# Kernel tuning notes

Hardware: AMD Instinct MI355X
Metric: run time of the kernel (lower is better)

Reference implementation:

```python
import jax, jax.numpy as jnp
import numpy as np

Nmax = 200
B = 512
LATENT = 128
ENC_H = 256
DEC_H = 512
M = 20


def setup_inputs() -> dict:
    key = jax.random.key(0)
    ks = jax.random.split(key, 16)

    def rn(k, shape):
        return jax.random.normal(k, shape, jnp.float32) / np.sqrt(shape[0]).astype(np.float32)

    inp = {}
    inp["x"] = jax.random.normal(ks[0], (Nmax + 1, B, 5), jnp.float32)
    inp["N_s"] = jax.random.randint(ks[1], (B, 1), 0, Nmax, jnp.int32)
    inp["eps"] = jax.random.normal(ks[2], (B, LATENT), jnp.float32)
    # bidirectional encoder LSTM (torch gate order i,f,g,o)
    inp["enc_Wih_f"] = rn(ks[3], (5, 4 * ENC_H))
    inp["enc_Whh_f"] = rn(ks[4], (ENC_H, 4 * ENC_H))
    inp["enc_b_f"] = jnp.zeros((4 * ENC_H,), jnp.float32)
    inp["enc_Wih_b"] = rn(ks[5], (5, 4 * ENC_H))
    inp["enc_Whh_b"] = rn(ks[6], (ENC_H, 4 * ENC_H))
    inp["enc_b_b"] = jnp.zeros((4 * ENC_H,), jnp.float32)
    inp["W_mu"] = rn(ks[7], (2 * ENC_H, LATENT))
    inp["b_mu"] = jnp.zeros((LATENT,), jnp.float32)
    inp["W_logvar"] = rn(ks[8], (2 * ENC_H, LATENT))
    inp["b_logvar"] = jnp.zeros((LATENT,), jnp.float32)
    # decoder
    inp["W_fc_in"] = rn(ks[9], (LATENT, 2 * DEC_H))
    inp["b_fc_in"] = jnp.zeros((2 * DEC_H,), jnp.float32)
    inp["dec_Wih"] = rn(ks[10], (5 + LATENT, 4 * DEC_H))
    inp["dec_Whh"] = rn(ks[11], (DEC_H, 4 * DEC_H))
    inp["dec_b"] = jnp.zeros((4 * DEC_H,), jnp.float32)
    inp["W_out"] = rn(ks[12], (DEC_H, 6 * M + 3))
    inp["b_out"] = jnp.zeros((6 * M + 3,), jnp.float32)
    return inp


def _lstm_step(h, c, x, Wih, Whh, b):
    g = x @ Wih + h @ Whh + b
    i, f, gg, o = jnp.split(g, 4, axis=-1)
    c = jax.nn.sigmoid(f) * c + jax.nn.sigmoid(i) * jnp.tanh(gg)
    h = jax.nn.sigmoid(o) * jnp.tanh(c)
    return h, c


def reference(x, N_s, eps, enc_Wih_f, enc_Whh_f, enc_b_f, enc_Wih_b, enc_Whh_b, enc_b_b,
              W_mu, b_mu, W_logvar, b_logvar, W_fc_in, b_fc_in,
              dec_Wih, dec_Whh, dec_b, W_out, b_out):
    Bn = x.shape[1]
    dt = x.dtype

    # ---- bidirectional LSTM encoder -> mean, logvar ----
    def run(xs, Wih, Whh, b):
        H = Whh.shape[0]
        def step(hc, xt):
            h, c = _lstm_step(hc[0], hc[1], xt, Wih, Whh, b)
            return (h, c), None
        (h, _), _ = jax.lax.scan(step, (jnp.zeros((Bn, H), dt), jnp.zeros((Bn, H), dt)), xs)
        return h

    h_enc = jnp.concatenate([run(x, enc_Wih_f, enc_Whh_f, enc_b_f),
                             run(x[::-1], enc_Wih_b, enc_Whh_b, enc_b_b)], axis=-1)
    mean = h_enc @ W_mu + b_mu
    logvar = h_enc @ W_logvar + b_logvar
    z = mean + jnp.exp(logvar / 2) * eps  # reparameterize

    # decoder initial state from z
    hc0 = jnp.tanh(z @ W_fc_in + b_fc_in)
    h0, c0 = jnp.split(hc0, 2, axis=-1)

    # ---- make_target ----
    lens = N_s[:, 0]  # [B]
    mask = (jnp.arange(Nmax + 1)[:, None] < lens[None, :]).astype(dt)  # [Nmax+1, B]
    dx, dy = x[..., 0], x[..., 1]

    stroke0 = jnp.broadcast_to(jnp.array([0, 0, 1, 0, 0], dt), (Bn, 5))  # SOS
    empty = jnp.array([0, 0, 0, 0, 1], dt)
    steps = jnp.arange(1, Nmax)
    xs = (x[1:Nmax], dx[1:Nmax], dy[1:Nmax], mask[1:Nmax], steps)

    def step(carry, inp):
        h, c, prev, pl, ol = carry
        xt, dxt, dyt, mt, i = inp
        h, c = _lstm_step(h, c, jnp.concatenate([prev, z], axis=-1), dec_Wih, dec_Whh, dec_b)
        y = h @ W_out + b_out  # [B, 6M+3]
        mix = y[:, :6 * M].reshape(Bn, M, 6)
        pi_h, mu_x, mu_y, sx_h, sy_h, rho_h = (mix[..., j] for j in range(6))
        q_h = y[:, 6 * M:]
        pi = jax.nn.softmax(pi_h, axis=-1)
        sx, sy, rho = jnp.exp(sx_h), jnp.exp(sy_h), jnp.tanh(rho_h)
        # pen reconstruction loss (categorical CE over p1,p2,p3)
        pl = pl + (-(xt[:, 2:] * jax.nn.log_softmax(q_h, axis=-1)).sum() / Bn) / Nmax
        # offset reconstruction loss (bivariate GMM NLL, masked)
        zx = (dxt[:, None] - mu_x) / sx
        zy = (dyt[:, None] - mu_y) / sy
        om = 1.0 - rho * rho
        pdf = jnp.exp(-(zx * zx + zy * zy - 2.0 * rho * zx * zy) / (2.0 * om)) / (2.0 * jnp.pi * sx * sy * jnp.sqrt(om))
        gmm = (pi * pdf).sum(axis=-1)
        ol = ol + (-(mt * jnp.log(gmm + 1e-6)).sum() / Bn) / Nmax
        # deterministic next stroke: expected offsets + argmax pen state
        q = jax.nn.softmax(q_h, axis=-1)
        stroke = jnp.concatenate([(pi * mu_x).sum(-1, keepdims=True),
                                  (pi * mu_y).sum(-1, keepdims=True),
                                  jax.nn.one_hot(jnp.argmax(q, axis=-1), 3, dtype=dt)], axis=-1)
        stroke = jnp.where((i > lens)[:, None], empty, stroke)  # per-index stroke masking
        return (h, c, stroke, pl, ol), stroke

    init = (h0, c0, stroke0, jnp.zeros((), dt), jnp.zeros((), dt))
    (_, _, _, pen_loss, offset_loss), strokes = jax.lax.scan(step, init, xs)
    # torch returns strokes[1:]; row Nmax is never written -> zeros
    strokes = jnp.concatenate([strokes, jnp.zeros((1, Bn, 5), dt)], axis=0)  # [Nmax, B, 5]
    return strokes, offset_loss, pen_loss, mean, logvar
```

## Files before the change

### kernel.cpp

```cpp
#include <hip/hip_runtime.h>
#include <hip/hip_bf16.h>
#include <math.h>

#define NMAX 200
#define BATCH 512
#define EH 256
#define DH 512
#define NMIX 20
#define HE_BLK 131072
#define HD_BLK 262144

typedef unsigned short u16;
typedef __bf16 bfx8 __attribute__((ext_vector_type(8)));
typedef float  fx4  __attribute__((ext_vector_type(4)));
typedef u16    us8  __attribute__((ext_vector_type(8)));

__device__ __forceinline__ float sigm(float x) { return 1.0f / (1.0f + __expf(-x)); }
__device__ __forceinline__ u16 f2bf(float x) {
    unsigned u = __float_as_uint(x);
    unsigned r = u + 0x7fffu + ((u >> 16) & 1u);
    return (u16)(r >> 16);
}
__device__ __forceinline__ float bf2f(u16 h) { return __uint_as_float(((unsigned)h) << 16); }

__device__ __forceinline__ int ldsidx(int r, int k) { return r * 64 + (k ^ ((r & 7) << 3)); }

__device__ __forceinline__ void stageA(u16* As, const u16* src, int stride) {
    int t = threadIdx.x;
    int r = t >> 3, k0 = (t & 7) * 8;
    *(us8*)&As[ldsidx(r, k0)] = *(const us8*)&src[r * stride + k0];
}
__device__ __forceinline__ void stageB(u16* Bs, const u16* wT, int K, int GS, int j0, int kbase) {
#pragma unroll
    for (int i = 0; i < 4; ++i) {
        int idx = i * 256 + threadIdx.x;
        int r = idx >> 3, k0 = (idx & 7) * 8;
        int n = (r >> 5) * GS + j0 + (r & 31);
        *(us8*)&Bs[ldsidx(r, k0)] = *(const us8*)&wT[n * K + kbase + k0];
    }
}

__device__ __forceinline__ void gemm_chunk(const u16* As_hi, const u16* As_lo,
                                           const u16* Bs_hi, const u16* Bs_lo,
                                           int wv, int lane, fx4 acc[2][2]) {
    const int ar = lane & 15, kg = (lane >> 4) * 8;
#pragma unroll
    for (int ks = 0; ks < 2; ++ks) {
        const int kk = ks * 32 + kg;
        bfx8 ah[2], al[2], bh[2], bl[2];
#pragma unroll
        for (int mt = 0; mt < 2; ++mt) {
            int r = mt * 16 + ar;
            int idx = ldsidx(r, kk);
            ah[mt] = *(const bfx8*)&As_hi[idx];
            al[mt] = *(const bfx8*)&As_lo[idx];
        }
#pragma unroll
        for (int nt = 0; nt < 2; ++nt) {
            int r = wv * 32 + nt * 16 + ar;
            int idx = ldsidx(r, kk);
            bh[nt] = *(const bfx8*)&Bs_hi[idx];
            bl[nt] = *(const bfx8*)&Bs_lo[idx];
        }
#pragma unroll
        for (int mt = 0; mt < 2; ++mt)
#pragma unroll
            for (int nt = 0; nt < 2; ++nt) {
                acc[mt][nt] = __builtin_amdgcn_mfma_f32_16x16x32_bf16(ah[mt], bh[nt], acc[mt][nt], 0, 0, 0);
                acc[mt][nt] = __builtin_amdgcn_mfma_f32_16x16x32_bf16(ah[mt], bl[nt], acc[mt][nt], 0, 0, 0);
                acc[mt][nt] = __builtin_amdgcn_mfma_f32_16x16x32_bf16(al[mt], bh[nt], acc[mt][nt], 0, 0, 0);
            }
    }
}

__global__ __launch_bounds__(256) void prep_split_T(const float* __restrict__ src,
                                                    u16* dhi, u16* dlo, int K, int Nsrc, int Nout) {
    int idx = blockIdx.x * 256 + threadIdx.x;
    if (idx >= Nout * K) return;
    int n = idx / K, k = idx - n * K;
    float v = (n < Nsrc) ? src[k * Nsrc + n] : 0.0f;
    u16 hh = f2bf(v);
    dhi[idx] = hh;
    dlo[idx] = f2bf(v - bf2f(hh));
}

__global__ __launch_bounds__(256) void enc_step_m(
    const float* __restrict__ x,
    const float* __restrict__ Wih_f, const float* __restrict__ b_f,
    const float* __restrict__ Wih_b, const float* __restrict__ b_b,
    const u16* whhT,
    u16* he,
    float* c_base,
    int t)
{
    const int dir = blockIdx.z;
    const int j0 = blockIdx.x * 32;
    const int row0 = blockIdx.y * 32;
    const int pb = t & 1, nb = pb ^ 1;
    const int ts = dir ? (NMAX - t) : t;
    const float* Wih  = dir ? Wih_b : Wih_f;
    const float* bias = dir ? b_b : b_f;
    const u16* wT_hi = whhT + (dir * 2 + 0) * 262144;
    const u16* wT_lo = whhT + (dir * 2 + 1) * 262144;
    const u16* hp_hi = he + ((pb * 2 + dir) * 2 + 0) * HE_BLK;
    const u16* hp_lo = he + ((pb * 2 + dir) * 2 + 1) * HE_BLK;
    u16* hn_hi = he + ((nb * 2 + dir) * 2 + 0) * HE_BLK;
    u16* hn_lo = he + ((nb * 2 + dir) * 2 + 1) * HE_BLK;
    float* c = c_base + dir * 131072;

    __shared__ __align__(16) char smem[40960];
    u16* As_hi = (u16*)smem;
    u16* As_lo = As_hi + 2048;
    u16* Bs_hi = As_lo + 2048;
    u16* Bs_lo = Bs_hi + 8192;
    float (*gL)[32][32] = (float(*)[32][32])(smem + 8192);
    __shared__ float xL[32][5];
    __shared__ float WihL[5][128];
    __shared__ float biasL[128];

    const int tid = threadIdx.x;
    const int wv = tid >> 6, lane = tid & 63;
    if (tid < 160) { int r = tid / 5, i = tid % 5; xL[r][i] = x[ts * 2560 + (row0 + r) * 5 + i]; }
    if (tid < 128) {
        biasL[tid] = bias[(tid >> 5) * 256 + j0 + (tid & 31)];
#pragma unroll
        for (int i = 0; i < 5; ++i) WihL[i][tid] = Wih[i * 1024 + (tid >> 5) * 256 + j0 + (tid & 31)];
    }

    fx4 acc[2][2] = {};
    for (int ch = 0; ch < 4; ++ch) {
        if (ch) __syncthreads();
        const int kb = ch * 64;
        stageA(As_hi, hp_hi + row0 * 256 + kb, 256);
        stageA(As_lo, hp_lo + row0 * 256 + kb, 256);
        stageB(Bs_hi, wT_hi, 256, 256, j0, kb);
        stageB(Bs_lo, wT_lo, 256, 256, j0, kb);
        __syncthreads();
        gemm_chunk(As_hi, As_lo, Bs_hi, Bs_lo, wv, lane, acc);
    }
    __syncthreads();
#pragma unroll
    for (int mt = 0; mt < 2; ++mt)
#pragma unroll
        for (int nt = 0; nt < 2; ++nt)
#pragma unroll
            for (int r2 = 0; r2 < 4; ++r2)
                gL[wv][mt * 16 + (lane >> 4) * 4 + r2][nt * 16 + (lane & 15)] = acc[mt][nt][r2];
    __syncthreads();

    {
        const int j = tid & 31, rq = tid >> 5;
#pragma unroll
        for (int ii = 0; ii < 4; ++ii) {
            const int b = rq + ii * 8;
            float gv[4];
#pragma unroll
            for (int g = 0; g < 4; ++g) {
                float s = gL[g][b][j] + biasL[g * 32 + j];
#pragma unroll
                for (int i = 0; i < 5; ++i) s += xL[b][i] * WihL[i][g * 32 + j];
                gv[g] = s;
            }
            const int gidx = (row0 + b) * 256 + j0 + j;
            float cv = c[gidx];
            cv = sigm(gv[1]) * cv + sigm(gv[0]) * tanhf(gv[2]);
            c[gidx] = cv;
            float hv = sigm(gv[3]) * tanhf(cv);
            u16 hh = f2bf(hv);
            hn_hi[gidx] = hh;
            hn_lo[gidx] = f2bf(hv - bf2f(hh));
        }
    }
}

__global__ __launch_bounds__(256) void latent1(
    const u16* he,
    const float* __restrict__ W_mu, const float* __restrict__ b_mu,
    const float* __restrict__ W_lv, const float* __restrict__ b_lv,
    const float* __restrict__ eps, float* z, float* out)
{
    __shared__ float hs[16 * 512];
    const int row0 = blockIdx.x * 16;
    const int tid = threadIdx.x;
    const u16* hf_hi = he + ((1 * 2 + 0) * 2 + 0) * HE_BLK;
    const u16* hf_lo = he + ((1 * 2 + 0) * 2 + 1) * HE_BLK;
    const u16* hb_hi = he + ((1 * 2 + 1) * 2 + 0) * HE_BLK;
    const u16* hb_lo = he + ((1 * 2 + 1) * 2 + 1) * HE_BLK;
    for (int i = tid; i < 8192; i += 256) {
        int r = i >> 9, col = i & 511;
        int gi = (row0 + r) * 256;
        float v;
        if (col < 256) v = bf2f(hf_hi[gi + col]) + bf2f(hf_lo[gi + col]);
        else { int cc = col - 256; v = bf2f(hb_hi[gi + cc]) + bf2f(hb_lo[gi + cc]); }
        hs[i] = v;
    }
    __syncthreads();
    for (int p = tid; p < 2048; p += 256) {
        int r = p >> 7, cc = p & 127;
        const float* hr = hs + r * 512;
        float m = 0, lv = 0;
#pragma unroll 8
        for (int k = 0; k < 512; ++k) {
            float hv = hr[k];
            m  += hv * W_mu[k * 128 + cc];
            lv += hv * W_lv[k * 128 + cc];
        }
        m += b_mu[cc]; lv += b_lv[cc];
        int b = row0 + r;
        out[512002 + b * 128 + cc] = m;
        out[577538 + b * 128 + cc] = lv;
        z[b * 128 + cc] = m + __expf(0.5f * lv) * eps[b * 128 + cc];
    }
}

__global__ __launch_bounds__(256) void latent2(
    const float* __restrict__ z, const float* __restrict__ W_fc, const float* __restrict__ b_fc,
    const float* __restrict__ dWih, const float* __restrict__ dec_b,
    u16* hd, float* c_d, float* zpre)
{
    __shared__ float zs[16 * 128];
    const int row0 = blockIdx.y * 16;
    const int tid = threadIdx.x;
    u16* h0_hi = hd + 0;
    u16* h0_lo = hd + HD_BLK;
    {
        float4* dst = (float4*)zs;
        const float4* src = (const float4*)(z + row0 * 128);
        for (int i = tid; i < 512; i += 256) dst[i] = src[i];
    }
    __syncthreads();
    const int colbase = blockIdx.x * 128;
    for (int p = tid; p < 16 * 128; p += 256) {
        int r = p >> 7, cl = p & 127;
        int col = colbase + cl;
        const float* zr = zs + r * 128;
        int b = row0 + r;
        if (col < 1024) {
            float acc = 0;
#pragma unroll 8
            for (int k = 0; k < 128; ++k) acc += zr[k] * W_fc[k * 1024 + col];
            float v = tanhf(acc + b_fc[col]);
            if (col < 512) {
                u16 hh = f2bf(v);
                h0_hi[b * 512 + col] = hh;
                h0_lo[b * 512 + col] = f2bf(v - bf2f(hh));
            } else c_d[b * 512 + (col - 512)] = v;
        } else {
            int n = col - 1024;
            float acc = 0;
#pragma unroll 8
            for (int k = 0; k < 128; ++k) acc += zr[k] * dWih[(5 + k) * 2048 + n];
            zpre[b * 2048 + n] = acc + dec_b[n];
        }
    }
}

template<int MODE>
__global__ __launch_bounds__(256) void dec_step_m(
    const float* __restrict__ x, const int* __restrict__ N_s,
    const float* __restrict__ dec_Wih, const float* __restrict__ b_out,
    const u16* whhT,
    const u16* woutT,
    const float* zpre,
    u16* hd,
    float* c_d, float* out, int s)
{
    const int j0 = blockIdx.x * 32;
    const int row0 = blockIdx.y * 32;
    const int pb = s & 1, nb = pb ^ 1;
    const u16* hp_hi = hd + (pb * 2 + 0) * HD_BLK;
    const u16* hp_lo = hd + (pb * 2 + 1) * HD_BLK;
    u16* hn_hi = hd + (nb * 2 + 0) * HD_BLK;
    u16* hn_lo = hd + (nb * 2 + 1) * HD_BLK;

    __shared__ __align__(16) char smem[40960];
    u16* As_hi = (u16*)smem;
    u16* As_lo = As_hi + 2048;
    u16* Bs_hi = As_lo + 2048;
    u16* Bs_lo = Bs_hi + 8192;
    float (*ysL)[128] = (float(*)[128])(smem + 8192);
    float (*gL)[32][32] = (float(*)[32][32])(smem + 8192);
    __shared__ float sxs[32][5];
    __shared__ float xtL[32][5];
    __shared__ float dwL[5][128];
    __shared__ float redL[64];

    const int tid = threadIdx.x;
    const int wv = tid >> 6, lane = tid & 63;

    if (MODE != 2 && tid < 128) {
#pragma unroll
        for (int i = 0; i < 5; ++i) dwL[i][tid] = dec_Wih[i * 2048 + (tid >> 5) * 512 + j0 + (tid & 31)];
    }
    if constexpr (MODE == 0) {
        if (tid < 160) { int r = tid / 5, i = tid % 5; sxs[r][i] = (i == 2) ? 1.0f : 0.0f; }
    } else {
        const int sy = s - 1;
        if (tid < 160) { int r = tid / 5, i = tid % 5; xtL[r][i] = x[(sy + 1) * 2560 + (row0 + r) * 5 + i]; }
        fx4 acc[2][2] = {};
        for (int ch = 0; ch < 8; ++ch) {
            if (ch) __syncthreads();
            const int kb = ch * 64;
            stageA(As_hi, hp_hi + row0 * 512 + kb, 512);
            stageA(As_lo, hp_lo + row0 * 512 + kb, 512);
            stageB(Bs_hi, woutT, 512, 32, 0, kb);
            stageB(Bs_lo, woutT + 65536, 512, 32, 0, kb);
            __syncthreads();
            gemm_chunk(As_hi, As_lo, Bs_hi, Bs_lo, wv, lane, acc);
        }
        __syncthreads();
#pragma unroll
        for (int mt = 0; mt < 2; ++mt)
#pragma unroll
            for (int nt = 0; nt < 2; ++nt)
#pragma unroll
                for (int r2 = 0; r2 < 4; ++r2) {
                    int bl = mt * 16 + (lane >> 4) * 4 + r2;
                    int col = wv * 32 + nt * 16 + (lane & 15);
                    ysL[bl][col] = acc[mt][nt][r2] + ((col < 123) ? b_out[col] : 0.0f);
                }
        __syncthreads();
        {
            const int row = tid >> 3, g = tid & 7;
            const float* yr = ysL[row];
            const float dx = xtL[row][0], dy = xtL[row][1];
            float pm = -1e30f;
            for (int cg = g; cg < NMIX; cg += 8) pm = fmaxf(pm, yr[cg * 6]);
            pm = fmaxf(pm, __shfl_xor(pm, 1));
            pm = fmaxf(pm, __shfl_xor(pm, 2));
            pm = fmaxf(pm, __shfl_xor(pm, 4));
            float S = 0, gp = 0, gx = 0, gy = 0;
            for (int cg = g; cg < NMIX; cg += 8) {
                float ph = yr[cg * 6], mux = yr[cg * 6 + 1], muy = yr[cg * 6 + 2];
                float ssx = __expf(yr[cg * 6 + 3]), ssy = __expf(yr[cg * 6 + 4]);
                float rho = tanhf(yr[cg * 6 + 5]);
                float e = __expf(ph - pm);
                float zx = (dx - mux) / ssx, zy = (dy - muy) / ssy;
                float om = 1.0f - rho * rho;
                float pdf = __expf(-(zx * zx + zy * zy - 2.0f * rho * zx * zy) / (2.0f * om))
                            * (0.15915494309189535f / (ssx * ssy * sqrtf(om)));
                S += e; gp += e * pdf; gx += e * mux; gy += e * muy;
            }
#pragma unroll
            for (int off = 1; off < 8; off <<= 1) {
                S += __shfl_xor(S, off); gp += __shfl_xor(gp, off);
                gx += __shfl_xor(gx, off); gy += __shfl_xor(gy, off);
            }
            if (g == 0) {
                const int b = row0 + row;
                float q0 = yr[120], q1 = yr[121], q2 = yr[122];
                float qm = fmaxf(q0, fmaxf(q1, q2));
                float lse = qm + logf(__expf(q0 - qm) + __expf(q1 - qm) + __expf(q2 - qm));
                float pl = -(xtL[row][2] * (q0 - lse) + xtL[row][3] * (q1 - lse) + xtL[row][4] * (q2 - lse));
                int len = N_s[b];
                float ol = ((sy + 1) < len) ? -logf(gp / S + 1e-6f) : 0.0f;
                int am = 0; float bv = q0;
                if (q1 > bv) { bv = q1; am = 1; }
                if (q2 > bv) { bv = q2; am = 2; }
                float s0, s1, s2, s3, s4;
                if ((sy + 1) > len) { s0 = s1 = s2 = s3 = 0.0f; s4 = 1.0f; }
                else { s0 = gx / S; s1 = gy / S; s2 = (am == 0); s3 = (am == 1); s4 = (am == 2); }
                sxs[row][0] = s0; sxs[row][1] = s1; sxs[row][2] = s2; sxs[row][3] = s3; sxs[row][4] = s4;
                if (blockIdx.x == 0) {
                    float* so = out + sy * 2560 + b * 5;
                    so[0] = s0; so[1] = s1; so[2] = s2; so[3] = s3; so[4] = s4;
                    redL[row] = pl; redL[32 + row] = ol;
                }
            }
        }
        __syncthreads();
        if (blockIdx.x == 0 && tid == 0) {
            float spl = 0, sol = 0;
            for (int r = 0; r < 32; ++r) { spl += redL[r]; sol += redL[32 + r]; }
            atomicAdd(out + 512001, spl * (1.0f / 102400.0f));
            atomicAdd(out + 512000, sol * (1.0f / 102400.0f));
        }
    }
    if constexpr (MODE == 2) return;

    __syncthreads();
    fx4 acc2[2][2] = {};
    for (int ch = 0; ch < 8; ++ch) {
        if (ch) __syncthreads();
        const int kb = ch * 64;
        stageA(As_hi, hp_hi + row0 * 512 + kb, 512);
        stageA(As_lo, hp_lo + row0 * 512 + kb, 512);
        stageB(Bs_hi, whhT, 512, 512, j0, kb);
        stageB(Bs_lo, whhT + 1048576, 512, 512, j0, kb);
        __syncthreads();
        gemm_chunk(As_hi, As_lo, Bs_hi, Bs_lo, wv, lane, acc2);
    }
    __syncthreads();
#pragma unroll
    for (int mt = 0; mt < 2; ++mt)
#pragma unroll
        for (int nt = 0; nt < 2; ++nt)
#pragma unroll
            for (int r2 = 0; r2 < 4; ++r2)
                gL[wv][mt * 16 + (lane >> 4) * 4 + r2][nt * 16 + (lane & 15)] = acc2[mt][nt][r2];
    __syncthreads();
    {
        const int j = tid & 31, rq = tid >> 5;
#pragma unroll
        for (int ii = 0; ii < 4; ++ii) {
            const int b = rq + ii * 8;
            const int gb = row0 + b;
            float gv[4];
#pragma unroll
            for (int g = 0; g < 4; ++g) {
                float sum = gL[g][b][j] + zpre[gb * 2048 + g * 512 + j0 + j];
#pragma unroll
                for (int i = 0; i < 5; ++i) sum += sxs[b][i] * dwL[i][g * 32 + j];
                gv[g] = sum;
            }
            const int gidx = gb * 512 + j0 + j;
            float cv = c_d[gidx];
            cv = sigm(gv[1]) * cv + sigm(gv[0]) * tanhf(gv[2]);
            c_d[gidx] = cv;
            float hv = sigm(gv[3]) * tanhf(cv);
            u16 hh = f2bf(hv);
            hn_hi[gidx] = hh;
            hn_lo[gidx] = f2bf(hv - bf2f(hh));
        }
    }
}

extern "C" void kernel_launch(void* const* d_in, const int* in_sizes, int n_in,
                              void* d_out_, int out_size, void* d_ws, size_t ws_size,
                              hipStream_t stream) {
    const float* x         = (const float*)d_in[0];
    const int*   N_s       = (const int*)  d_in[1];
    const float* eps       = (const float*)d_in[2];
    const float* enc_Wih_f = (const float*)d_in[3];
    const float* enc_Whh_f = (const float*)d_in[4];
    const float* enc_b_f   = (const float*)d_in[5];
    const float* enc_Wih_b = (const float*)d_in[6];
    const float* enc_Whh_b = (const float*)d_in[7];
    const float* enc_b_b   = (const float*)d_in[8];
    const float* W_mu      = (const float*)d_in[9];
    const float* b_mu      = (const float*)d_in[10];
    const float* W_logvar  = (const float*)d_in[11];
    const float* b_logvar  = (const float*)d_in[12];
    const float* W_fc_in   = (const float*)d_in[13];
    const float* b_fc_in   = (const float*)d_in[14];
    const float* dec_Wih   = (const float*)d_in[15];
    const float* dec_Whh   = (const float*)d_in[16];
    const float* dec_b     = (const float*)d_in[17];
    const float* W_out     = (const float*)d_in[18];
    const float* b_out     = (const float*)d_in[19];
    float* out = (float*)d_out_;
    float* ws  = (float*)d_ws;

    float* c_f  = ws;
    float* c_d  = ws + 262144;
    float* zpre = ws + 524288;
    float* z    = ws + 1572864;
    u16* U     = (u16*)(ws + 1638400);
    u16* he    = U;
    u16* hd    = U + 1048576;
    u16* encT  = U + 2097152;
    u16* decT  = U + 3145728;
    u16* woutT = U + 5242880;

    hipMemsetAsync(c_f, 0, 262144 * sizeof(float), stream);
    hipMemsetAsync(he, 0, 4 * HE_BLK * sizeof(u16), stream);
    hipMemsetAsync(out + 509440, 0, 2562 * sizeof(float), stream);

    prep_split_T<<<1024, 256, 0, stream>>>(enc_Whh_f, encT,           encT + 262144,  256, 1024, 1024);
    prep_split_T<<<1024, 256, 0, stream>>>(enc_Whh_b, encT + 524288,  encT + 786432,  256, 1024, 1024);
    prep_split_T<<<4096, 256, 0, stream>>>(dec_Whh,   decT,           decT + 1048576, 512, 2048, 2048);
    prep_split_T<<<256,  256, 0, stream>>>(W_out,     woutT,          woutT + 65536,  512, 123, 128);

    for (int t = 0; t <= NMAX; ++t)
        enc_step_m<<<dim3(8, 16, 2), 256, 0, stream>>>(
            x, enc_Wih_f, enc_b_f, enc_Wih_b, enc_b_b, encT, he, c_f, t);

    latent1<<<32, 256, 0, stream>>>(he, W_mu, b_mu, W_logvar, b_logvar, eps, z, out);
    latent2<<<dim3(24, 32), 256, 0, stream>>>(z, W_fc_in, b_fc_in, dec_Wih, dec_b, hd, c_d, zpre);

    dec_step_m<0><<<dim3(16, 16), 256, 0, stream>>>(x, N_s, dec_Wih, b_out, decT, woutT, zpre, hd, c_d, out, 0);
    for (int s = 1; s <= NMAX - 2; ++s)
        dec_step_m<1><<<dim3(16, 16), 256, 0, stream>>>(x, N_s, dec_Wih, b_out, decT, woutT, zpre, hd, c_d, out, s);
    dec_step_m<2><<<dim3(1, 16), 256, 0, stream>>>(x, N_s, dec_Wih, b_out, decT, woutT, zpre, hd, c_d, out, NMAX - 1);
}
```

Before: 6.356 ms.

## Replace per-step LSTM launches with persistent kernels using row-group barriers

The roughly 400 per-timestep launches for the encoder and decoder are replaced by two persistent kernels of 256 blocks each. Each kernel loops over time and synchronises only the blocks that share a batch row tile, through atomic counter barriers in global memory. Cell state and input weights now stay in registers instead of round-tripping through global memory. The decoder output projection is split across the 16 column blocks, staged through a global ybuf, and joined by an extra barrier, so the old redundant full W_out GEMM runs once rather than in every block. The code assumes all 256 blocks are co-resident; if they are not, the spin barriers deadlock.

Measured after the change: 9.065 ms. 1.43x slower.

```diff
diff --git a/kernel.cpp b/kernel.cpp
--- a/kernel.cpp
+++ b/kernel.cpp
@@ -3,7 +3,6 @@
 #include <math.h>
 
 #define NMAX 200
-#define BATCH 512
 #define EH 256
 #define DH 512
 #define NMIX 20
@@ -39,6 +38,13 @@
         *(us8*)&Bs[ldsidx(r, k0)] = *(const us8*)&wT[n * K + kbase + k0];
     }
 }
+__device__ __forceinline__ void stageY(u16* Ys, const u16* wT, int nbase, int kb) {
+    int t = threadIdx.x;
+    if (t < 128) {
+        int r = t >> 3, k0 = (t & 7) * 8;
+        *(us8*)&Ys[ldsidx(r, k0)] = *(const us8*)&wT[(nbase + r) * 512 + kb + k0];
+    }
+}
 
 __device__ __forceinline__ void gemm_chunk(const u16* As_hi, const u16* As_lo,
                                            const u16* Bs_hi, const u16* Bs_lo,
@@ -50,15 +56,13 @@
         bfx8 ah[2], al[2], bh[2], bl[2];
 #pragma unroll
         for (int mt = 0; mt < 2; ++mt) {
-            int r = mt * 16 + ar;
-            int idx = ldsidx(r, kk);
+            int idx = ldsidx(mt * 16 + ar, kk);
             ah[mt] = *(const bfx8*)&As_hi[idx];
             al[mt] = *(const bfx8*)&As_lo[idx];
         }
 #pragma unroll
         for (int nt = 0; nt < 2; ++nt) {
-            int r = wv * 32 + nt * 16 + ar;
-            int idx = ldsidx(r, kk);
+            int idx = ldsidx(wv * 32 + nt * 16 + ar, kk);
             bh[nt] = *(const bfx8*)&Bs_hi[idx];
             bl[nt] = *(const bfx8*)&Bs_lo[idx];
         }
@@ -71,6 +75,25 @@
                 acc[mt][nt] = __builtin_amdgcn_mfma_f32_16x16x32_bf16(al[mt], bh[nt], acc[mt][nt], 0, 0, 0);
             }
     }
+}
+
+__device__ __forceinline__ void group_bar(unsigned* bar, unsigned nb) {
+    __syncthreads();
+    if (threadIdx.x == 0) {
+        unsigned* cnt = bar;
+        unsigned* gen = bar + 1;
+        unsigned g = __hip_atomic_load(gen, __ATOMIC_RELAXED, __HIP_MEMORY_SCOPE_AGENT);
+        unsigned old = __hip_atomic_fetch_add(cnt, 1u, __ATOMIC_ACQ_REL, __HIP_MEMORY_SCOPE_AGENT);
+        if (old == nb - 1) {
+            __hip_atomic_store(cnt, 0u, __ATOMIC_RELAXED, __HIP_MEMORY_SCOPE_AGENT);
+            __hip_atomic_fetch_add(gen, 1u, __ATOMIC_RELEASE, __HIP_MEMORY_SCOPE_AGENT);
+        } else {
+            while (__hip_atomic_load(gen, __ATOMIC_RELAXED, __HIP_MEMORY_SCOPE_AGENT) == g)
+                __builtin_amdgcn_s_sleep(2);
+            (void)__hip_atomic_load(gen, __ATOMIC_ACQUIRE, __HIP_MEMORY_SCOPE_AGENT);
+        }
+    }
+    __syncthreads();
 }
 
 __global__ __launch_bounds__(256) void prep_split_T(const float* __restrict__ src,
@@ -84,29 +107,22 @@
     dlo[idx] = f2bf(v - bf2f(hh));
 }
 
-__global__ __launch_bounds__(256) void enc_step_m(
+__global__ __launch_bounds__(256) void enc_persist(
     const float* __restrict__ x,
     const float* __restrict__ Wih_f, const float* __restrict__ b_f,
     const float* __restrict__ Wih_b, const float* __restrict__ b_b,
-    const u16* whhT,
-    u16* he,
-    float* c_base,
-    int t)
+    const u16* __restrict__ whhT, u16* __restrict__ he,
+    unsigned* __restrict__ bar)
 {
-    const int dir = blockIdx.z;
-    const int j0 = blockIdx.x * 32;
-    const int row0 = blockIdx.y * 32;
-    const int pb = t & 1, nb = pb ^ 1;
-    const int ts = dir ? (NMAX - t) : t;
+    const int bx = blockIdx.x;
+    const int dir = bx >> 7, jx = (bx >> 4) & 7, rt = bx & 15;
+    const int j0 = jx * 32, row0 = rt * 32;
+    unsigned* mybar = bar + (dir * 16 + rt) * 32;
+
     const float* Wih  = dir ? Wih_b : Wih_f;
     const float* bias = dir ? b_b : b_f;
     const u16* wT_hi = whhT + (dir * 2 + 0) * 262144;
     const u16* wT_lo = whhT + (dir * 2 + 1) * 262144;
-    const u16* hp_hi = he + ((pb * 2 + dir) * 2 + 0) * HE_BLK;
-    const u16* hp_lo = he + ((pb * 2 + dir) * 2 + 1) * HE_BLK;
-    u16* hn_hi = he + ((nb * 2 + dir) * 2 + 0) * HE_BLK;
-    u16* hn_lo = he + ((nb * 2 + dir) * 2 + 1) * HE_BLK;
-    float* c = c_base + dir * 131072;
 
     __shared__ __align__(16) char smem[40960];
     u16* As_hi = (u16*)smem;
@@ -115,61 +131,71 @@
     u16* Bs_lo = Bs_hi + 8192;
     float (*gL)[32][32] = (float(*)[32][32])(smem + 8192);
     __shared__ float xL[32][5];
-    __shared__ float WihL[5][128];
-    __shared__ float biasL[128];
 
     const int tid = threadIdx.x;
     const int wv = tid >> 6, lane = tid & 63;
-    if (tid < 160) { int r = tid / 5, i = tid % 5; xL[r][i] = x[ts * 2560 + (row0 + r) * 5 + i]; }
-    if (tid < 128) {
-        biasL[tid] = bias[(tid >> 5) * 256 + j0 + (tid & 31)];
-#pragma unroll
-        for (int i = 0; i < 5; ++i) WihL[i][tid] = Wih[i * 1024 + (tid >> 5) * 256 + j0 + (tid & 31)];
-    }
-
-    fx4 acc[2][2] = {};
-    for (int ch = 0; ch < 4; ++ch) {
-        if (ch) __syncthreads();
-        const int kb = ch * 64;
-        stageA(As_hi, hp_hi + row0 * 256 + kb, 256);
-        stageA(As_lo, hp_lo + row0 * 256 + kb, 256);
-        stageB(Bs_hi, wT_hi, 256, 256, j0, kb);
-        stageB(Bs_lo, wT_lo, 256, 256, j0, kb);
+    const int j = tid & 31, rq = tid >> 5;
+
+    float wih[5][4], bi4[4];
+#pragma unroll
+    for (int g = 0; g < 4; ++g) {
+        bi4[g] = bias[g * 256 + j0 + j];
+#pragma unroll
+        for (int i = 0; i < 5; ++i) wih[i][g] = Wih[i * 1024 + g * 256 + j0 + j];
+    }
+    float c4[4] = {0.f, 0.f, 0.f, 0.f};
+
+    for (int t = 0; t <= NMAX; ++t) {
+        const int pb = t & 1, nb = pb ^ 1;
+        const int ts = dir ? (NMAX - t) : t;
+        const u16* hp_hi = he + ((pb * 2 + dir) * 2 + 0) * HE_BLK;
+        const u16* hp_lo = he + ((pb * 2 + dir) * 2 + 1) * HE_BLK;
+        u16* hn_hi = he + ((nb * 2 + dir) * 2 + 0) * HE_BLK;
+        u16* hn_lo = he + ((nb * 2 + dir) * 2 + 1) * HE_BLK;
+
+        if (tid < 160) xL[tid / 5][tid % 5] = x[ts * 2560 + (row0 + tid / 5) * 5 + tid % 5];
+
+        fx4 acc[2][2] = {};
+        for (int ch = 0; ch < 4; ++ch) {
+            if (ch) __syncthreads();
+            const int kb = ch * 64;
+            stageA(As_hi, hp_hi + row0 * 256 + kb, 256);
+            stageA(As_lo, hp_lo + row0 * 256 + kb, 256);
+            stageB(Bs_hi, wT_hi, 256, 256, j0, kb);
+            stageB(Bs_lo, wT_lo, 256, 256, j0, kb);
+            __syncthreads();
+            gemm_chunk(As_hi, As_lo, Bs_hi, Bs_lo, wv, lane, acc);
+        }
         __syncthreads();
-        gemm_chunk(As_hi, As_lo, Bs_hi, Bs_lo, wv, lane, acc);
-    }
-    __syncthreads();
-#pragma unroll
-    for (int mt = 0; mt < 2; ++mt)
-#pragma unroll
-        for (int nt = 0; nt < 2; ++nt)
-#pragma unroll
-            for (int r2 = 0; r2 < 4; ++r2)
-                gL[wv][mt * 16 + (lane >> 4) * 4 + r2][nt * 16 + (lane & 15)] = acc[mt][nt][r2];
-    __syncthreads();
-
-    {
-        const int j = tid & 31, rq = tid >> 5;
+#pragma unroll
+        for (int mt = 0; mt < 2; ++mt)
+#pragma unroll
+            for (int nt = 0; nt < 2; ++nt)
+#pragma unroll
+                for (int r2 = 0; r2 < 4; ++r2)
+                    gL[wv][mt * 16 + (lane >> 4) * 4 + r2][nt * 16 + (lane & 15)] = acc[mt][nt][r2];
+        __syncthreads();
 #pragma unroll
         for (int ii = 0; ii < 4; ++ii) {
             const int b = rq + ii * 8;
             float gv[4];
 #pragma unroll
             for (int g = 0; g < 4; ++g) {
-                float s = gL[g][b][j] + biasL[g * 32 + j];
-#pragma unroll
-                for (int i = 0; i < 5; ++i) s += xL[b][i] * WihL[i][g * 32 + j];
-                gv[g] = s;
-            }
+                float s2 = gL[g][b][j] + bi4[g];
+#pragma unroll
+                for (int i = 0; i < 5; ++i) s2 += xL[b][i] * wih[i][g];
+                gv[g] = s2;
+            }
+            float cv = c4[ii];
+            cv = sigm(gv[1]) * cv + sigm(gv[0]) * tanhf(gv[2]);
+            c4[ii] = cv;
+            float hv = sigm(gv[3]) * tanhf(cv);
             const int gidx = (row0 + b) * 256 + j0 + j;
-            float cv = c[gidx];
-            cv = sigm(gv[1]) * cv + sigm(gv[0]) * tanhf(gv[2]);
-            c[gidx] = cv;
-            float hv = sigm(gv[3]) * tanhf(cv);
             u16 hh = f2bf(hv);
             hn_hi[gidx] = hh;
             hn_lo[gidx] = f2bf(hv - bf2f(hh));
         }
+        group_bar(mybar, 8u);
     }
 }
 
@@ -255,172 +281,206 @@
     }
 }
 
-template<int MODE>
-__global__ __launch_bounds__(256) void dec_step_m(
+__global__ __launch_bounds__(256) void dec_persist(
     const float* __restrict__ x, const int* __restrict__ N_s,
     const float* __restrict__ dec_Wih, const float* __restrict__ b_out,
-    const u16* whhT,
-    const u16* woutT,
-    const float* zpre,
-    u16* hd,
-    float* c_d, float* out, int s)
+    const u16* __restrict__ whhT, const u16* __restrict__ woutT,
+    const float* __restrict__ zpre, u16* __restrict__ hd,
+    const float* __restrict__ c_init, float* __restrict__ ybuf,
+    float* __restrict__ out, unsigned* __restrict__ bar)
 {
-    const int j0 = blockIdx.x * 32;
-    const int row0 = blockIdx.y * 32;
-    const int pb = s & 1, nb = pb ^ 1;
-    const u16* hp_hi = hd + (pb * 2 + 0) * HD_BLK;
-    const u16* hp_lo = hd + (pb * 2 + 1) * HD_BLK;
-    u16* hn_hi = hd + (nb * 2 + 0) * HD_BLK;
-    u16* hn_lo = hd + (nb * 2 + 1) * HD_BLK;
-
-    __shared__ __align__(16) char smem[40960];
+    const int bx = blockIdx.x;
+    const int jx = bx >> 4, rt = bx & 15;
+    const int j0 = jx * 32, row0 = rt * 32;
+    unsigned* mybar = bar + (32 + rt) * 32;
+    const int ysbase = (jx * 8 > 112) ? 112 : jx * 8;
+    const int wlo = jx * 8, whi = (jx * 8 + 8 < 123) ? jx * 8 + 8 : 123;
+
+    const u16* whh_hi = whhT;
+    const u16* whh_lo = whhT + 1048576;
+    const u16* wo_hi  = woutT;
+    const u16* wo_lo  = woutT + 65536;
+
+    __shared__ __align__(16) char smem[46080];
     u16* As_hi = (u16*)smem;
     u16* As_lo = As_hi + 2048;
     u16* Bs_hi = As_lo + 2048;
     u16* Bs_lo = Bs_hi + 8192;
-    float (*ysL)[128] = (float(*)[128])(smem + 8192);
-    float (*gL)[32][32] = (float(*)[32][32])(smem + 8192);
-    __shared__ float sxs[32][5];
-    __shared__ float xtL[32][5];
-    __shared__ float dwL[5][128];
-    __shared__ float redL[64];
+    u16* yBhi  = Bs_lo + 8192;
+    u16* yBlo  = yBhi + 1024;
+    float (*gL)[32][32]   = (float(*)[32][32])(smem + 8192);
+    float (*yred)[32][16] = (float(*)[32][16])(smem);
+    __shared__ float xtL[32][5], sxs[32][5], redL[64];
+    __shared__ int lenL[32];
 
     const int tid = threadIdx.x;
     const int wv = tid >> 6, lane = tid & 63;
-
-    if (MODE != 2 && tid < 128) {
-#pragma unroll
-        for (int i = 0; i < 5; ++i) dwL[i][tid] = dec_Wih[i * 2048 + (tid >> 5) * 512 + j0 + (tid & 31)];
-    }
-    if constexpr (MODE == 0) {
-        if (tid < 160) { int r = tid / 5, i = tid % 5; sxs[r][i] = (i == 2) ? 1.0f : 0.0f; }
-    } else {
-        const int sy = s - 1;
-        if (tid < 160) { int r = tid / 5, i = tid % 5; xtL[r][i] = x[(sy + 1) * 2560 + (row0 + r) * 5 + i]; }
+    const int j = tid & 31, rq = tid >> 5;
+
+    float dw[5][4];
+#pragma unroll
+    for (int g = 0; g < 4; ++g)
+#pragma unroll
+        for (int i = 0; i < 5; ++i) dw[i][g] = dec_Wih[i * 2048 + g * 512 + j0 + j];
+    float c4[4];
+#pragma unroll
+    for (int ii = 0; ii < 4; ++ii) c4[ii] = c_init[(row0 + rq + ii * 8) * 512 + j0 + j];
+    if (tid < 32) lenL[tid] = N_s[row0 + tid];
+    if (tid < 160) sxs[tid / 5][tid % 5] = (tid % 5 == 2) ? 1.0f : 0.0f;
+
+    for (int s = 0; s <= 199; ++s) {
+        const bool do_y = (s > 0), do_cell = (s < 199);
+        const int pb = s & 1, nb = pb ^ 1;
+        const u16* hp_hi = hd + (pb * 2 + 0) * HD_BLK;
+        const u16* hp_lo = hd + (pb * 2 + 1) * HD_BLK;
+        u16* hn_hi = hd + (nb * 2 + 0) * HD_BLK;
+        u16* hn_lo = hd + (nb * 2 + 1) * HD_BLK;
+
+        if (do_y && tid < 160) xtL[tid / 5][tid % 5] = x[s * 2560 + (row0 + tid / 5) * 5 + tid % 5];
+
         fx4 acc[2][2] = {};
+        fx4 accy[2] = {};
         for (int ch = 0; ch < 8; ++ch) {
             if (ch) __syncthreads();
             const int kb = ch * 64;
             stageA(As_hi, hp_hi + row0 * 512 + kb, 512);
             stageA(As_lo, hp_lo + row0 * 512 + kb, 512);
-            stageB(Bs_hi, woutT, 512, 32, 0, kb);
-            stageB(Bs_lo, woutT + 65536, 512, 32, 0, kb);
+            if (do_cell) {
+                stageB(Bs_hi, whh_hi, 512, 512, j0, kb);
+                stageB(Bs_lo, whh_lo, 512, 512, j0, kb);
+            }
+            if (do_y) {
+                stageY(yBhi, wo_hi, ysbase, kb);
+                stageY(yBlo, wo_lo, ysbase, kb);
+            }
             __syncthreads();
-            gemm_chunk(As_hi, As_lo, Bs_hi, Bs_lo, wv, lane, acc);
+            if (do_cell) gemm_chunk(As_hi, As_lo, Bs_hi, Bs_lo, wv, lane, acc);
+            if (do_y && wv < 2) {
+                const int ar = lane & 15, kg = (lane >> 4) * 8;
+                const int kk = wv * 32 + kg;
+                bfx8 ybh = *(const bfx8*)&yBhi[ldsidx(ar, kk)];
+                bfx8 ybl = *(const bfx8*)&yBlo[ldsidx(ar, kk)];
+#pragma unroll
+                for (int mt = 0; mt < 2; ++mt) {
+                    int idx = ldsidx(mt * 16 + ar, kk);
+                    bfx8 ah = *(const bfx8*)&As_hi[idx];
+                    bfx8 al = *(const bfx8*)&As_lo[idx];
+                    accy[mt] = __builtin_amdgcn_mfma_f32_16x16x32_bf16(ah, ybh, accy[mt], 0, 0, 0);
+                    accy[mt] = __builtin_amdgcn_mfma_f32_16x16x32_bf16(ah, ybl, accy[mt], 0, 0, 0);
+                    accy[mt] = __builtin_amdgcn_mfma_f32_16x16x32_bf16(al, ybh, accy[mt], 0, 0, 0);
+                }
+            }
         }
         __syncthreads();
-#pragma unroll
-        for (int mt = 0; mt < 2; ++mt)
-#pragma unroll
-            for (int nt = 0; nt < 2; ++nt)
-#pragma unroll
-                for (int r2 = 0; r2 < 4; ++r2) {
-                    int bl = mt * 16 + (lane >> 4) * 4 + r2;
-                    int col = wv * 32 + nt * 16 + (lane & 15);
-                    ysL[bl][col] = acc[mt][nt][r2] + ((col < 123) ? b_out[col] : 0.0f);
+
+        if (do_y) {
+            if (wv < 2) {
+#pragma unroll
+                for (int mt = 0; mt < 2; ++mt)
+#pragma unroll
+                    for (int r2 = 0; r2 < 4; ++r2)
+                        yred[wv][mt * 16 + (lane >> 4) * 4 + r2][lane & 15] = accy[mt][r2];
+            }
+            __syncthreads();
+            for (int e = tid; e < 512; e += 256) {
+                int r = e >> 4, cl = e & 15;
+                int col = ysbase + cl;
+                if (col >= wlo && col < whi) {
+                    float v = yred[0][r][cl] + yred[1][r][cl] + b_out[col];
+                    ybuf[(row0 + r) * 128 + col] = v;
                 }
-        __syncthreads();
-        {
-            const int row = tid >> 3, g = tid & 7;
-            const float* yr = ysL[row];
-            const float dx = xtL[row][0], dy = xtL[row][1];
-            float pm = -1e30f;
-            for (int cg = g; cg < NMIX; cg += 8) pm = fmaxf(pm, yr[cg * 6]);
-            pm = fmaxf(pm, __shfl_xor(pm, 1));
-            pm = fmaxf(pm, __shfl_xor(pm, 2));
-            pm = fmaxf(pm, __shfl_xor(pm, 4));
-            float S = 0, gp = 0, gx = 0, gy = 0;
-            for (int cg = g; cg < NMIX; cg += 8) {
-                float ph = yr[cg * 6], mux = yr[cg * 6 + 1], muy = yr[cg * 6 + 2];
-                float ssx = __expf(yr[cg * 6 + 3]), ssy = __expf(yr[cg * 6 + 4]);
-                float rho = tanhf(yr[cg * 6 + 5]);
-                float e = __expf(ph - pm);
-                float zx = (dx - mux) / ssx, zy = (dy - muy) / ssy;
-                float om = 1.0f - rho * rho;
-                float pdf = __expf(-(zx * zx + zy * zy - 2.0f * rho * zx * zy) / (2.0f * om))
-                            * (0.15915494309189535f / (ssx * ssy * sqrtf(om)));
-                S += e; gp += e * pdf; gx += e * mux; gy += e * muy;
-            }
-#pragma unroll
-            for (int off = 1; off < 8; off <<= 1) {
-                S += __shfl_xor(S, off); gp += __shfl_xor(gp, off);
-                gx += __shfl_xor(gx, off); gy += __shfl_xor(gy, off);
-            }
-            if (g == 0) {
-                const int b = row0 + row;
-                float q0 = yr[120], q1 = yr[121], q2 = yr[122];
-                float qm = fmaxf(q0, fmaxf(q1, q2));
-                float lse = qm + logf(__expf(q0 - qm) + __expf(q1 - qm) + __expf(q2 - qm));
-                float pl = -(xtL[row][2] * (q0 - lse) + xtL[row][3] * (q1 - lse) + xtL[row][4] * (q2 - lse));
-                int len = N_s[b];
-                float ol = ((sy + 1) < len) ? -logf(gp / S + 1e-6f) : 0.0f;
-                int am = 0; float bv = q0;
-                if (q1 > bv) { bv = q1; am = 1; }
-                if (q2 > bv) { bv = q2; am = 2; }
-                float s0, s1, s2, s3, s4;
-                if ((sy + 1) > len) { s0 = s1 = s2 = s3 = 0.0f; s4 = 1.0f; }
-                else { s0 = gx / S; s1 = gy / S; s2 = (am == 0); s3 = (am == 1); s4 = (am == 2); }
-                sxs[row][0] = s0; sxs[row][1] = s1; sxs[row][2] = s2; sxs[row][3] = s3; sxs[row][4] = s4;
-                if (blockIdx.x == 0) {
-                    float* so = out + sy * 2560 + b * 5;
-                    so[0] = s0; so[1] = s1; so[2] = s2; so[3] = s3; so[4] = s4;
-                    redL[row] = pl; redL[32 + row] = ol;
+            }
+            group_bar(mybar, 16u);
+            {
+                const int row = tid >> 3, g = tid & 7;
+                const float* yr = ybuf + (row0 + row) * 128;
+                const float dxv = xtL[row][0], dyv = xtL[row][1];
+                float pm = -1e30f;
+                for (int cg = g; cg < NMIX; cg += 8) pm = fmaxf(pm, yr[cg * 6]);
+                pm = fmaxf(pm, __shfl_xor(pm, 1));
+                pm = fmaxf(pm, __shfl_xor(pm, 2));
+                pm = fmaxf(pm, __shfl_xor(pm, 4));
+                float S = 0, gp = 0, gx = 0, gy = 0;
+                for (int cg = g; cg < NMIX; cg += 8) {
+                    float ph = yr[cg * 6], mux = yr[cg * 6 + 1], muy = yr[cg * 6 + 2];
+                    float ssx = __expf(yr[cg * 6 + 3]), ssy = __expf(yr[cg * 6 + 4]);
+                    float rho = tanhf(yr[cg * 6 + 5]);
+                    float e = __expf(ph - pm);
+                    float zx = (dxv - mux) / ssx, zy = (dyv - muy) / ssy;
+                    float om = 1.0f - rho * rho;
+                    float pdf = __expf(-(zx * zx + zy * zy - 2.0f * rho * zx * zy) / (2.0f * om))
+                                * (0.15915494309189535f / (ssx * ssy * sqrtf(om)));
+                    S += e; gp += e * pdf; gx += e * mux; gy += e * muy;
                 }
-            }
-        }
-        __syncthreads();
-        if (blockIdx.x == 0 && tid == 0) {
-            float spl = 0, sol = 0;
-            for (int r = 0; r < 32; ++r) { spl += redL[r]; sol += redL[32 + r]; }
-            atomicAdd(out + 512001, spl * (1.0f / 102400.0f));
-            atomicAdd(out + 512000, sol * (1.0f / 102400.0f));
-        }
-    }
-    if constexpr (MODE == 2) return;
-
-    __syncthreads();
-    fx4 acc2[2][2] = {};
-    for (int ch = 0; ch < 8; ++ch) {
-        if (ch) __syncthreads();
-        const int kb = ch * 64;
-        stageA(As_hi, hp_hi + row0 * 512 + kb, 512);
-        stageA(As_lo, hp_lo + row0 * 512 + kb, 512);
-        stageB(Bs_hi, whhT, 512, 512, j0, kb);
-        stageB(Bs_lo, whhT + 1048576, 512, 512, j0, kb);
-        __syncthreads();
-        gemm_chunk(As_hi, As_lo, Bs_hi, Bs_lo, wv, lane, acc2);
-    }
-    __syncthreads();
-#pragma unroll
-    for (int mt = 0; mt < 2; ++mt)
-#pragma unroll
-        for (int nt = 0; nt < 2; ++nt)
-#pragma unroll
-            for (int r2 = 0; r2 < 4; ++r2)
-                gL[wv][mt * 16 + (lane >> 4) * 4 + r2][nt * 16 + (lane & 15)] = acc2[mt][nt][r2];
-    __syncthreads();
-    {
-        const int j = tid & 31, rq = tid >> 5;
-#pragma unroll
-        for (int ii = 0; ii < 4; ++ii) {
-            const int b = rq + ii * 8;
-            const int gb = row0 + b;
-            float gv[4];
-#pragma unroll
-            for (int g = 0; g < 4; ++g) {
-                float sum = gL[g][b][j] + zpre[gb * 2048 + g * 512 + j0 + j];
-#pragma unroll
-                for (int i = 0; i < 5; ++i) sum += sxs[b][i] * dwL[i][g * 32 + j];
-                gv[g] = sum;
-            }
-            const int gidx = gb * 512 + j0 + j;
-            float cv = c_d[gidx];
-            cv = sigm(gv[1]) * cv + sigm(gv[0]) * tanhf(gv[2]);
-            c_d[gidx] = cv;
-            float hv = sigm(gv[3]) * tanhf(cv);
-            u16 hh = f2bf(hv);
-            hn_hi[gidx] = hh;
-            hn_lo[gidx] = f2bf(hv - bf2f(hh));
+#pragma unroll
+                for (int off = 1; off < 8; off <<= 1) {
+                    S += __shfl_xor(S, off); gp += __shfl_xor(gp, off);
+                    gx += __shfl_xor(gx, off); gy += __shfl_xor(gy, off);
+                }
+                if (g == 0) {
+                    const int b = row0 + row;
+                    const int sy = s - 1;
+                    float q0 = yr[120], q1 = yr[121], q2 = yr[122];
+                    int len = lenL[row];
+                    int am = 0; float bv = q0;
+                    if (q1 > bv) { bv = q1; am = 1; }
+                    if (q2 > bv) { bv = q2; am = 2; }
+                    float s0, s1, s2, s3, s4;
+                    if ((sy + 1) > len) { s0 = s1 = s2 = s3 = 0.0f; s4 = 1.0f; }
+                    else { s0 = gx / S; s1 = gy / S; s2 = (am == 0); s3 = (am == 1); s4 = (am == 2); }
+                    sxs[row][0] = s0; sxs[row][1] = s1; sxs[row][2] = s2; sxs[row][3] = s3; sxs[row][4] = s4;
+                    if (jx == 0) {
+                        float qm = fmaxf(q0, fmaxf(q1, q2));
+                        float lse = qm + logf(__expf(q0 - qm) + __expf(q1 - qm) + __expf(q2 - qm));
+                        float pl = -(xtL[row][2] * (q0 - lse) + xtL[row][3] * (q1 - lse) + xtL[row][4] * (q2 - lse));
+                        float ol = ((sy + 1) < len) ? -logf(gp / S + 1e-6f) : 0.0f;
+                        float* so = out + sy * 2560 + b * 5;
+                        so[0] = s0; so[1] = s1; so[2] = s2; so[3] = s3; so[4] = s4;
+                        redL[row] = pl; redL[32 + row] = ol;
+                    }
+                }
+            }
+            __syncthreads();
+            if (jx == 0 && tid == 0) {
+                float spl = 0, sol = 0;
+                for (int r = 0; r < 32; ++r) { spl += redL[r]; sol += redL[32 + r]; }
+                atomicAdd(out + 512001, spl * (1.0f / 102400.0f));
+                atomicAdd(out + 512000, sol * (1.0f / 102400.0f));
+            }
+        }
+
+        if (do_cell) {
+            __syncthreads();
+#pragma unroll
+            for (int mt = 0; mt < 2; ++mt)
+#pragma unroll
+                for (int nt = 0; nt < 2; ++nt)
+#pragma unroll
+                    for (int r2 = 0; r2 < 4; ++r2)
+                        gL[wv][mt * 16 + (lane >> 4) * 4 + r2][nt * 16 + (lane & 15)] = acc[mt][nt][r2];
+            __syncthreads();
+#pragma unroll
+            for (int ii = 0; ii < 4; ++ii) {
+                const int b = rq + ii * 8;
+                const int gb = row0 + b;
+                float gv[4];
+#pragma unroll
+                for (int g = 0; g < 4; ++g) {
+                    float sum = gL[g][b][j] + zpre[gb * 2048 + g * 512 + j0 + j];
+#pragma unroll
+                    for (int i = 0; i < 5; ++i) sum += sxs[b][i] * dw[i][g];
+                    gv[g] = sum;
+                }
+                float cv = c4[ii];
+                cv = sigm(gv[1]) * cv + sigm(gv[0]) * tanhf(gv[2]);
+                c4[ii] = cv;
+                float hv = sigm(gv[3]) * tanhf(cv);
+                const int gidx = gb * 512 + j0 + j;
+                u16 hh = f2bf(hv);
+                hn_hi[gidx] = hh;
+                hn_lo[gidx] = f2bf(hv - bf2f(hh));
+            }
+            group_bar(mybar, 16u);
         }
     }
 }
@@ -451,19 +511,20 @@
     float* out = (float*)d_out_;
     float* ws  = (float*)d_ws;
 
-    float* c_f  = ws;
-    float* c_d  = ws + 262144;
-    float* zpre = ws + 524288;
-    float* z    = ws + 1572864;
-    u16* U     = (u16*)(ws + 1638400);
+    float* c_d   = ws + 0;
+    float* zpre  = ws + 262144;
+    float* z     = ws + 1310720;
+    float* ybuf  = ws + 1376256;
+    unsigned* bar = (unsigned*)(ws + 1441792);
+    u16* U     = (u16*)(ws + 1443840);
     u16* he    = U;
     u16* hd    = U + 1048576;
     u16* encT  = U + 2097152;
     u16* decT  = U + 3145728;
     u16* woutT = U + 5242880;
 
-    hipMemsetAsync(c_f, 0, 262144 * sizeof(float), stream);
     hipMemsetAsync(he, 0, 4 * HE_BLK * sizeof(u16), stream);
+    hipMemsetAsync(bar, 0, 1536 * sizeof(unsigned), stream);
     hipMemsetAsync(out + 509440, 0, 2562 * sizeof(float), stream);
 
     prep_split_T<<<1024, 256, 0, stream>>>(enc_Whh_f, encT,           encT + 262144,  256, 1024, 1024);
@@ -471,15 +532,8 @@
     prep_split_T<<<4096, 256, 0, stream>>>(dec_Whh,   decT,           decT + 1048576, 512, 2048, 2048);
     prep_split_T<<<256,  256, 0, stream>>>(W_out,     woutT,          woutT + 65536,  512, 123, 128);
 
-    for (int t = 0; t <= NMAX; ++t)
-        enc_step_m<<<dim3(8, 16, 2), 256, 0, stream>>>(
-            x, enc_Wih_f, enc_b_f, enc_Wih_b, enc_b_b, encT, he, c_f, t);
-
+    enc_persist<<<256, 256, 0, stream>>>(x, enc_Wih_f, enc_b_f, enc_Wih_b, enc_b_b, encT, he, bar);
     latent1<<<32, 256, 0, stream>>>(he, W_mu, b_mu, W_logvar, b_logvar, eps, z, out);
     latent2<<<dim3(24, 32), 256, 0, stream>>>(z, W_fc_in, b_fc_in, dec_Wih, dec_b, hd, c_d, zpre);
-
-    dec_step_m<0><<<dim3(16, 16), 256, 0, stream>>>(x, N_s, dec_Wih, b_out, decT, woutT, zpre, hd, c_d, out, 0);
-    for (int s = 1; s <= NMAX - 2; ++s)
-        dec_step_m<1><<<dim3(16, 16), 256, 0, stream>>>(x, N_s, dec_Wih, b_out, decT, woutT, zpre, hd, c_d, out, s);
-    dec_step_m<2><<<dim3(1, 16), 256, 0, stream>>>(x, N_s, dec_Wih, b_out, decT, woutT, zpre, hd, c_d, out, NMAX - 1);
-}
+    dec_persist<<<256, 256, 0, stream>>>(x, N_s, dec_Wih, b_out, decT, woutT, zpre, hd, c_d, ybuf, out, bar);
+}
```
